# Kernel optimization log

Hardware: AMD Instinct MI355X
Metric: run time of the kernel (lower is better)

Reference implementation:

```python
import jax, jax.numpy as jnp
import numpy as np

D_MODEL = 1024
NUM_HEADS = 16
D_K = D_MODEL // NUM_HEADS
LOCAL_WINDOW = 16
LOCALITY_STRENGTH = 2.0


def _xavier(key, shape):
    fan_in, fan_out = shape[1], shape[0]
    a = jnp.sqrt(6.0 / (fan_in + fan_out))
    return jax.random.uniform(key, shape, jnp.float32, -a, a)


def setup_inputs() -> dict:
    key = jax.random.key(0)
    ks = jax.random.split(key, 9)
    B, S = 4, 2048
    query = jax.random.normal(ks[0], (B, S, D_MODEL), jnp.float32)
    key_t = jax.random.normal(ks[1], (B, S, D_MODEL), jnp.float32)
    value = jax.random.normal(ks[2], (B, S, D_MODEL), jnp.float32)
    wq = _xavier(ks[3], (D_MODEL, D_MODEL))
    wk = _xavier(ks[4], (D_MODEL, D_MODEL))
    wv = _xavier(ks[5], (D_MODEL, D_MODEL))
    wo = _xavier(ks[6], (D_MODEL, D_MODEL))
    bq = jnp.zeros((D_MODEL,), jnp.float32)
    bk = jnp.zeros((D_MODEL,), jnp.float32)
    bv = jnp.zeros((D_MODEL,), jnp.float32)
    bo = jnp.zeros((D_MODEL,), jnp.float32)
    # learned local relative-position bias, length 2*W+1; randomize so grads/math are nontrivial
    local_bias = 0.02 * jax.random.normal(ks[7], (2 * LOCAL_WINDOW + 1,), jnp.float32)
    return {"query": query, "key": key_t, "value": value,
            "wq": wq, "bq": bq, "wk": wk, "bk": bk, "wv": wv, "bv": bv,
            "wo": wo, "bo": bo, "local_bias": local_bias}


def _local_bias_matrix(local_bias, seq_len):
    # bias[i, j] = local_bias[j - i + W] if |j - i| <= W else 0  (banded)
    i = jnp.arange(seq_len)
    rel = i[None, :] - i[:, None]                 # [S, S]
    valid = jnp.abs(rel) <= LOCAL_WINDOW
    idx = jnp.clip(rel + LOCAL_WINDOW, 0, 2 * LOCAL_WINDOW)
    return jnp.where(valid, local_bias[idx], 0.0)  # [S, S]


def reference(query, key, value, wq, bq, wk, bk, wv, bv, wo, bo, local_bias):
    B, S, _ = query.shape
    H, Dk = NUM_HEADS, D_K
    q = (query @ wq.T + bq).reshape(B, S, H, Dk).transpose(0, 2, 1, 3)  # [B,H,S,Dk]
    k = (key @ wk.T + bk).reshape(B, S, H, Dk).transpose(0, 2, 1, 3)
    v = (value @ wv.T + bv).reshape(B, S, H, Dk).transpose(0, 2, 1, 3)
    scores = jnp.einsum('bhqd,bhkd->bhqk', q, k) / jnp.sqrt(jnp.float32(Dk))
    bias = _local_bias_matrix(local_bias, S)       # [S,S], broadcasts over [B,H]
    scores = scores + LOCALITY_STRENGTH * bias
    attn = jax.nn.softmax(scores, axis=-1)
    out = jnp.einsum('bhqk,bhkd->bhqd', attn, v)   # [B,H,S,Dk]
    out = out.transpose(0, 2, 1, 3).reshape(B, S, H * Dk)
    return out @ wo.T + bo
```

## Files before the change

kernel.cpp:

```cpp
#include <hip/hip_runtime.h>
#include <hip/hip_bf16.h>
#include <stdint.h>

typedef __bf16 bf16_t;
typedef bf16_t bf16x8 __attribute__((ext_vector_type(8)));
typedef bf16_t bf16x4 __attribute__((ext_vector_type(4)));
typedef float f32x4 __attribute__((ext_vector_type(4)));

#define LOG2E 1.44269504088896340736f

__device__ __forceinline__ void gld16(const void* g, void* l) {
  __builtin_amdgcn_global_load_lds(
      (__attribute__((address_space(1))) void*)(void*)(g),
      (__attribute__((address_space(3))) void*)(l), 16, 0, 0);
}

__device__ __forceinline__ int swz(int byteoff) {
  return byteoff ^ (((byteoff >> 7) & 7) << 4);
}

__global__ __launch_bounds__(256) void cvt7_kernel(
    const float* __restrict__ a0, const float* __restrict__ a1, const float* __restrict__ a2,
    const float* __restrict__ w0, const float* __restrict__ w1,
    const float* __restrict__ w2, const float* __restrict__ w3,
    bf16_t* __restrict__ e0, bf16_t* __restrict__ e1, bf16_t* __restrict__ e2,
    bf16_t* __restrict__ f0, bf16_t* __restrict__ f1,
    bf16_t* __restrict__ f2, bf16_t* __restrict__ f3) {
  const float* s;
  bf16_t* d;
  int i, stride;
  if (blockIdx.x < 3072) {
    const int t = blockIdx.x >> 10;
    s = (t == 0) ? a0 : ((t == 1) ? a1 : a2);
    d = (t == 0) ? e0 : ((t == 1) ? e1 : e2);
    i = (blockIdx.x & 1023) * 256 + threadIdx.x;
    stride = 1024 * 256;
  } else {
    const int b = blockIdx.x - 3072;
    const int t = b >> 7;
    s = (t == 0) ? w0 : ((t == 1) ? w1 : ((t == 2) ? w2 : w3));
    d = (t == 0) ? f0 : ((t == 1) ? f1 : ((t == 2) ? f2 : f3));
    i = (b & 127) * 256 + threadIdx.x;
    stride = 128 * 256;
  }
#pragma unroll
  for (int u = 0; u < 8; ++u, i += stride) {
    const float4 v = reinterpret_cast<const float4*>(s)[i];
    bf16x4 o;
    o[0] = (bf16_t)v.x; o[1] = (bf16_t)v.y; o[2] = (bf16_t)v.z; o[3] = (bf16_t)v.w;
    reinterpret_cast<bf16x4*>(d)[i] = o;
  }
}

#define GBM 128
#define GBN 128
#define GBK 64

__device__ __forceinline__ void gemm_core(
    const bf16_t* __restrict__ A, const bf16_t* __restrict__ W,
    bf16_t* As, bf16_t* Bs, int m0, int n0, int K,
    int wm, int wn, int rr, int kk8, f32x4 acc[4][4]) {
  const int tid = threadIdx.x;
  const int t16 = tid * 16;
  int srow[4], scb[4];
#pragma unroll
  for (int i = 0; i < 4; ++i) {
    const int so = swz(i * 4096 + t16);
    srow[i] = so >> 7;
    scb[i] = so & 127;
  }
  const char* Ab = (const char*)A;
  const char* Wb = (const char*)W;
  const int nk = K / GBK;

#define GSTAGE(bufsel, kk0)                                                    \
  {                                                                            \
    char* Al = (char*)As + (bufsel) * 16384 + t16;                             \
    char* Bl = (char*)Bs + (bufsel) * 16384 + t16;                             \
    _Pragma("unroll")                                                          \
    for (int i = 0; i < 4; ++i) {                                              \
      gld16(Ab + ((size_t)(m0 + srow[i]) * K + (kk0)) * 2 + scb[i], Al + i * 4096); \
      gld16(Wb + ((size_t)(n0 + srow[i]) * K + (kk0)) * 2 + scb[i], Bl + i * 4096); \
    }                                                                          \
  }

  GSTAGE(0, 0)
  for (int t = 0; t < nk; ++t) {
    const int b = t & 1;
    asm volatile("s_waitcnt vmcnt(0)" ::: "memory");
    __builtin_amdgcn_s_barrier();
    __builtin_amdgcn_sched_barrier(0);
    GSTAGE(b ^ 1, ((t + 1) & (nk - 1)) * GBK)
    const char* Abl = (const char*)As + b * 16384;
    const char* Bbl = (const char*)Bs + b * 16384;
#pragma unroll
    for (int kk = 0; kk < 2; ++kk) {
      bf16x8 a[4], bb[4];
#pragma unroll
      for (int i = 0; i < 4; ++i)
        a[i] = *reinterpret_cast<const bf16x8*>(
            Abl + swz((wm + i * 16 + rr) * 128 + (kk * 32 + kk8) * 2));
#pragma unroll
      for (int i = 0; i < 4; ++i)
        bb[i] = *reinterpret_cast<const bf16x8*>(
            Bbl + swz((wn + i * 16 + rr) * 128 + (kk * 32 + kk8) * 2));
      __builtin_amdgcn_s_setprio(1);
#pragma unroll
      for (int i = 0; i < 4; ++i)
#pragma unroll
        for (int j = 0; j < 4; ++j)
          acc[i][j] = __builtin_amdgcn_mfma_f32_16x16x32_bf16(a[i], bb[j], acc[i][j], 0, 0, 0);
      __builtin_amdgcn_s_setprio(0);
    }
  }
#undef GSTAGE
}

__global__ __launch_bounds__(256) void gemm_qkv(
    const bf16_t* __restrict__ Xq, const bf16_t* __restrict__ Xk, const bf16_t* __restrict__ Xv,
    const bf16_t* __restrict__ Wq, const bf16_t* __restrict__ Wk, const bf16_t* __restrict__ Wv,
    const float* __restrict__ bq, const float* __restrict__ bk, const float* __restrict__ bv,
    bf16_t* __restrict__ Qo, bf16_t* __restrict__ Ko, bf16_t* __restrict__ Vo,
    int M, int N, int K) {
  const int z = blockIdx.z;
  const bf16_t* A = (z == 0) ? Xq : ((z == 1) ? Xk : Xv);
  const bf16_t* W = (z == 0) ? Wq : ((z == 1) ? Wk : Wv);
  const float* bias = (z == 0) ? bq : ((z == 1) ? bk : bv);
  bf16_t* Out = (z == 0) ? Qo : ((z == 1) ? Ko : Vo);

  __shared__ bf16_t As[2 * GBM * GBK];
  __shared__ bf16_t Bs[2 * GBN * GBK];
  const int tid = threadIdx.x;
  const int lane = tid & 63;
  const int w = tid >> 6;
  const int m0 = blockIdx.x * GBM;
  const int n0 = blockIdx.y * GBN;
  const int wm = (w >> 1) * 64;
  const int wn = (w & 1) * 64;
  const int rr = lane & 15;
  const int kk8 = (lane >> 4) * 8;

  f32x4 acc[4][4] = {};
  gemm_core(A, W, As, Bs, m0, n0, K, wm, wn, rr, kk8, acc);

  const int rg = (lane >> 4) * 4;
#pragma unroll
  for (int i = 0; i < 4; ++i) {
#pragma unroll
    for (int j = 0; j < 4; ++j) {
      const int col = n0 + wn + j * 16 + rr;
      const float bi = bias[col];
      if (z == 2) {
        const int row0 = m0 + wm + i * 16 + rg;
        const int b_ = row0 >> 11, s_ = row0 & 2047;
        const int h_ = col >> 6, d_ = col & 63;
        const int k64 = s_ & 63;
        const int sl = (k64 & 32) | ((k64 & 12) << 1) | ((k64 & 16) >> 2);
        const int scol = (s_ & ~63) | sl;
        bf16x4 pack;
#pragma unroll
        for (int r = 0; r < 4; ++r) pack[r] = (bf16_t)(acc[i][j][r] + bi);
        *reinterpret_cast<bf16x4*>(&Out[((size_t)((b_ * 16 + h_) * 64 + d_)) * 2048 + scol]) = pack;
      } else {
        const float scale = (z == 0) ? (0.125f * LOG2E) : 1.0f;
#pragma unroll
        for (int r = 0; r < 4; ++r) {
          const int row = m0 + wm + i * 16 + rg + r;
          const int b_ = row >> 11, s_ = row & 2047;
          const int h_ = col >> 6, d_ = col & 63;
          Out[((size_t)((b_ * 16 + h_) * 2048 + s_)) * 64 + d_] = (bf16_t)((acc[i][j][r] + bi) * scale);
        }
      }
    }
  }
}

__global__ __launch_bounds__(256) void gemm_o(
    const bf16_t* __restrict__ A, const bf16_t* __restrict__ W,
    const float* __restrict__ bias, float* __restrict__ Out,
    int M, int N, int K) {
  __shared__ bf16_t As[2 * GBM * GBK];
  __shared__ bf16_t Bs[2 * GBN * GBK];
  const int tid = threadIdx.x;
  const int lane = tid & 63;
  const int w = tid >> 6;
  const int m0 = blockIdx.x * GBM;
  const int n0 = blockIdx.y * GBN;
  const int wm = (w >> 1) * 64;
  const int wn = (w & 1) * 64;
  const int rr = lane & 15;
  const int kk8 = (lane >> 4) * 8;

  f32x4 acc[4][4] = {};
  gemm_core(A, W, As, Bs, m0, n0, K, wm, wn, rr, kk8, acc);

  const int rg = (lane >> 4) * 4;
#pragma unroll
  for (int i = 0; i < 4; ++i)
#pragma unroll
    for (int j = 0; j < 4; ++j) {
      const int col = n0 + wn + j * 16 + rr;
      const float bi = bias[col];
#pragma unroll
      for (int r = 0; r < 4; ++r) {
        const int row = m0 + wm + i * 16 + rg + r;
        Out[(size_t)row * N + col] = acc[i][j][r] + bi;
      }
    }
}

#define QT 256
#define KT 64

__global__ __launch_bounds__(256, 2) void attn_kernel(
    const bf16_t* __restrict__ Qg, const bf16_t* __restrict__ Kg,
    const bf16_t* __restrict__ Vtg, const float* __restrict__ lb,
    bf16_t* __restrict__ Og) {
  const int S = 2048;
  __shared__ bf16_t Qs[QT * 64];
  __shared__ bf16_t Ks[KT * 64];
  __shared__ bf16_t Vts[64 * KT];
  __shared__ float lbs[33];

  const int tid = threadIdx.x, lane = tid & 63, w = tid >> 6;
  const int bh = blockIdx.x;
  const int qt0 = blockIdx.y * QT;
  const int b_ = bh >> 4, h_ = bh & 15;

  const char* Qb = (const char*)(Qg + (size_t)bh * S * 64);
  const char* Kb = (const char*)(Kg + (size_t)bh * S * 64);
  const char* Vtb = (const char*)(Vtg + (size_t)bh * 64 * S);

#pragma unroll
  for (int i = 0; i < 8; ++i) {
    const int off = i * 4096 + tid * 16;
    gld16(Qb + (size_t)qt0 * 128 + swz(off), (char*)Qs + off);
  }
  if (tid < 33) lbs[tid] = lb[tid];

  const int L0 = tid * 16;
  const int W0 = swz(L0), W1 = swz(L0 + 4096);
  const int vd0 = L0 >> 7, vcb = L0 & 127;
  int4 kr0, kr1, vr0, vr1;

#define LOADKV(t)                                                              \
  {                                                                            \
    const char* kp = Kb + (size_t)(t) * 8192;                                  \
    kr0 = *reinterpret_cast<const int4*>(kp + L0);                             \
    kr1 = *reinterpret_cast<const int4*>(kp + L0 + 4096);                      \
    const char* vp = Vtb + (size_t)(t) * 128;                                  \
    vr0 = *reinterpret_cast<const int4*>(vp + (size_t)vd0 * 4096 + vcb);       \
    vr1 = *reinterpret_cast<const int4*>(vp + (size_t)(vd0 + 32) * 4096 + vcb);\
  }
#define WRITEKV()                                                              \
  {                                                                            \
    *reinterpret_cast<int4*>((char*)Ks + W0) = kr0;                            \
    *reinterpret_cast<int4*>((char*)Ks + W1) = kr1;                            \
    *reinterpret_cast<int4*>((char*)Vts + W0) = vr0;                           \
    *reinterpret_cast<int4*>((char*)Vts + W1) = vr1;                           \
  }

  LOADKV(0)
  __syncthreads();

  const int rr = lane & 15;
  const int kk8 = (lane >> 4) * 8;
  const int rg = (lane >> 4) * 4;

  bf16x8 qf[4][2];
#pragma unroll
  for (int qg = 0; qg < 4; ++qg)
#pragma unroll
    for (int kk = 0; kk < 2; ++kk) {
      const int off = (w * 64 + qg * 16 + rr) * 128 + (kk * 32 + kk8) * 2;
      qf[qg][kk] = *reinterpret_cast<const bf16x8*>((const char*)Qs + swz(off));
    }

  f32x4 oacc[4][4] = {};
  float lrowp[4] = {0.f, 0.f, 0.f, 0.f};

  for (int kt = 0; kt < S / KT; ++kt) {
    WRITEKV()
    __syncthreads();
    LOADKV((kt + 1) & 31)

    bf16x8 kf[4][2];
#pragma unroll
    for (int ni = 0; ni < 4; ++ni)
#pragma unroll
      for (int kk = 0; kk < 2; ++kk) {
        const int off = (ni * 16 + rr) * 128 + (kk * 32 + kk8) * 2;
        kf[ni][kk] = *reinterpret_cast<const bf16x8*>((const char*)Ks + swz(off));
      }
    bf16x8 vf[2][4];
#pragma unroll
    for (int kk = 0; kk < 2; ++kk)
#pragma unroll
      for (int nd = 0; nd < 4; ++nd) {
        const int off = (nd * 16 + rr) * 128 + (kk * 32 + kk8) * 2;
        vf[kk][nd] = *reinterpret_cast<const bf16x8*>((const char*)Vts + swz(off));
      }

    const int kbase = kt * KT;
#pragma unroll
    for (int qg = 0; qg < 4; ++qg) {
      f32x4 sc[4];
      __builtin_amdgcn_s_setprio(1);
#pragma unroll
      for (int ni = 0; ni < 4; ++ni) {
        f32x4 z = {0.f, 0.f, 0.f, 0.f};
#pragma unroll
        for (int kk = 0; kk < 2; ++kk)
          z = __builtin_amdgcn_mfma_f32_16x16x32_bf16(kf[ni][kk], qf[qg][kk], z, 0, 0, 0);
        sc[ni] = z;
      }
      __builtin_amdgcn_s_setprio(0);

      const int qlo = qt0 + w * 64 + qg * 16;
      if (kbase + KT + 16 > qlo && kbase < qlo + 16 + 16) {
        const int q = qlo + rr;
#pragma unroll
        for (int ni = 0; ni < 4; ++ni)
#pragma unroll
          for (int r = 0; r < 4; ++r) {
            const int rel = (kbase + ni * 16 + rg + r) - q;
            if (rel >= -16 && rel <= 16)
              sc[ni][r] += (2.0f * LOG2E) * lbs[rel + 16];
          }
      }

      bf16x8 paf[2];
      float ps0 = 0.f, ps1 = 0.f;
#pragma unroll
      for (int ni = 0; ni < 4; ++ni) {
        const float p0 = __builtin_amdgcn_exp2f(sc[ni][0]);
        const float p1 = __builtin_amdgcn_exp2f(sc[ni][1]);
        const float p2 = __builtin_amdgcn_exp2f(sc[ni][2]);
        const float p3 = __builtin_amdgcn_exp2f(sc[ni][3]);
        ps0 += p0 + p2;
        ps1 += p1 + p3;
        paf[ni >> 1][(ni & 1) * 4 + 0] = (bf16_t)p0;
        paf[ni >> 1][(ni & 1) * 4 + 1] = (bf16_t)p1;
        paf[ni >> 1][(ni & 1) * 4 + 2] = (bf16_t)p2;
        paf[ni >> 1][(ni & 1) * 4 + 3] = (bf16_t)p3;
      }
      lrowp[qg] += ps0 + ps1;

      __builtin_amdgcn_s_setprio(1);
#pragma unroll
      for (int kk = 0; kk < 2; ++kk)
#pragma unroll
        for (int nd = 0; nd < 4; ++nd)
          oacc[qg][nd] = __builtin_amdgcn_mfma_f32_16x16x32_bf16(paf[kk], vf[kk][nd], oacc[qg][nd], 0, 0, 0);
      __builtin_amdgcn_s_setprio(0);
    }
    __syncthreads();
  }

#pragma unroll
  for (int qg = 0; qg < 4; ++qg) {
    float t = lrowp[qg];
    t += __shfl_xor(t, 16, 64);
    t += __shfl_xor(t, 32, 64);
    float lf[4];
#pragma unroll
    for (int r = 0; r < 4; ++r)
      lf[r] = __shfl(t, (lane & 48) | (rg + r), 64);
#pragma unroll
    for (int nd = 0; nd < 4; ++nd)
#pragma unroll
      for (int r = 0; r < 4; ++r) {
        const int srow = qt0 + w * 64 + qg * 16 + rg + r;
        const int d = nd * 16 + rr;
        const float v = oacc[qg][nd][r] / lf[r];
        Og[((size_t)(b_ * 2048 + srow)) * 1024 + h_ * 64 + d] = (bf16_t)v;
      }
  }
}

extern "C" void kernel_launch(void* const* d_in, const int* in_sizes, int n_in,
                              void* d_out, int out_size, void* d_ws, size_t ws_size,
                              hipStream_t stream) {
  const float* q32 = (const float*)d_in[0];
  const float* k32 = (const float*)d_in[1];
  const float* v32 = (const float*)d_in[2];
  const float* wq = (const float*)d_in[3];
  const float* bq = (const float*)d_in[4];
  const float* wk = (const float*)d_in[5];
  const float* bk = (const float*)d_in[6];
  const float* wv = (const float*)d_in[7];
  const float* bv = (const float*)d_in[8];
  const float* wo = (const float*)d_in[9];
  const float* bo = (const float*)d_in[10];
  const float* lb = (const float*)d_in[11];

  const int M = 8192, N = 1024, K = 1024;
  const size_t REG = (size_t)M * N * 2;

  char* ws = (char*)d_ws;
  bf16_t* Xq = (bf16_t*)(ws + 0 * REG);
  bf16_t* Xk = (bf16_t*)(ws + 1 * REG);
  bf16_t* Xv = (bf16_t*)(ws + 2 * REG);
  bf16_t* Qb = (bf16_t*)(ws + 3 * REG);
  bf16_t* Wqb = (bf16_t*)(ws + 4 * REG);
  bf16_t* Wkb = Wqb + (size_t)N * K;
  bf16_t* Wvb = Wkb + (size_t)N * K;
  bf16_t* Wob = Wvb + (size_t)N * K;
  bf16_t* Kb = Xq;
  bf16_t* Vt = Xk;
  bf16_t* attn = Xv;

  cvt7_kernel<<<dim3(3584), dim3(256), 0, stream>>>(
      q32, k32, v32, wq, wk, wv, wo, Xq, Xk, Xv, Wqb, Wkb, Wvb, Wob);

  gemm_qkv<<<dim3(M / GBM, N / GBN, 3), 256, 0, stream>>>(
      Xq, Xk, Xv, Wqb, Wkb, Wvb, bq, bk, bv, Qb, Kb, Vt, M, N, K);

  attn_kernel<<<dim3(64, 2048 / QT), 256, 0, stream>>>(Qb, Kb, Vt, lb, attn);

  gemm_o<<<dim3(M / GBM, N / GBN), 256, 0, stream>>>(attn, Wob, bo, (float*)d_out, M, N, K);
}
```

Before: 196.0 us.

## Fuse fp32-to-bf16 activation conversion into QKV GEMM A-tile loading

The separate conversion pass over the three fp32 activation tensors is removed. The QKV GEMM now loads fp32 A tiles into registers, converts them to bf16 and writes them to swizzled LDS, while W tiles still arrive via global_load_lds. This avoids writing and re-reading roughly 48MB of bf16 intermediates, but each GEMM block reads twice the A bytes, and the register-staged loads add VGPR pressure and a synchronous wait per k-step.

```diff
diff --git a/kernel.cpp b/kernel.cpp
--- a/kernel.cpp
+++ b/kernel.cpp
@@ -19,32 +19,17 @@
   return byteoff ^ (((byteoff >> 7) & 7) << 4);
 }
 
-__global__ __launch_bounds__(256) void cvt7_kernel(
-    const float* __restrict__ a0, const float* __restrict__ a1, const float* __restrict__ a2,
-    const float* __restrict__ w0, const float* __restrict__ w1,
-    const float* __restrict__ w2, const float* __restrict__ w3,
-    bf16_t* __restrict__ e0, bf16_t* __restrict__ e1, bf16_t* __restrict__ e2,
-    bf16_t* __restrict__ f0, bf16_t* __restrict__ f1,
-    bf16_t* __restrict__ f2, bf16_t* __restrict__ f3) {
-  const float* s;
-  bf16_t* d;
-  int i, stride;
-  if (blockIdx.x < 3072) {
-    const int t = blockIdx.x >> 10;
-    s = (t == 0) ? a0 : ((t == 1) ? a1 : a2);
-    d = (t == 0) ? e0 : ((t == 1) ? e1 : e2);
-    i = (blockIdx.x & 1023) * 256 + threadIdx.x;
-    stride = 1024 * 256;
-  } else {
-    const int b = blockIdx.x - 3072;
-    const int t = b >> 7;
-    s = (t == 0) ? w0 : ((t == 1) ? w1 : ((t == 2) ? w2 : w3));
-    d = (t == 0) ? f0 : ((t == 1) ? f1 : ((t == 2) ? f2 : f3));
-    i = (b & 127) * 256 + threadIdx.x;
-    stride = 128 * 256;
-  }
-#pragma unroll
-  for (int u = 0; u < 8; ++u, i += stride) {
+__global__ __launch_bounds__(256) void cvt4_kernel(
+    const float* __restrict__ s0, const float* __restrict__ s1,
+    const float* __restrict__ s2, const float* __restrict__ s3,
+    bf16_t* __restrict__ d0, bf16_t* __restrict__ d1,
+    bf16_t* __restrict__ d2, bf16_t* __restrict__ d3) {
+  const int t = blockIdx.x >> 7;
+  const float* s = (t == 0) ? s0 : ((t == 1) ? s1 : ((t == 2) ? s2 : s3));
+  bf16_t* d = (t == 0) ? d0 : ((t == 1) ? d1 : ((t == 2) ? d2 : d3));
+  int i = (blockIdx.x & 127) * 256 + threadIdx.x;
+#pragma unroll
+  for (int u = 0; u < 8; ++u, i += 128 * 256) {
     const float4 v = reinterpret_cast<const float4*>(s)[i];
     bf16x4 o;
     o[0] = (bf16_t)v.x; o[1] = (bf16_t)v.y; o[2] = (bf16_t)v.z; o[3] = (bf16_t)v.w;
@@ -117,13 +102,13 @@
 }
 
 __global__ __launch_bounds__(256) void gemm_qkv(
-    const bf16_t* __restrict__ Xq, const bf16_t* __restrict__ Xk, const bf16_t* __restrict__ Xv,
+    const float* __restrict__ Xq, const float* __restrict__ Xk, const float* __restrict__ Xv,
     const bf16_t* __restrict__ Wq, const bf16_t* __restrict__ Wk, const bf16_t* __restrict__ Wv,
     const float* __restrict__ bq, const float* __restrict__ bk, const float* __restrict__ bv,
     bf16_t* __restrict__ Qo, bf16_t* __restrict__ Ko, bf16_t* __restrict__ Vo,
     int M, int N, int K) {
   const int z = blockIdx.z;
-  const bf16_t* A = (z == 0) ? Xq : ((z == 1) ? Xk : Xv);
+  const float* A = (z == 0) ? Xq : ((z == 1) ? Xk : Xv);
   const bf16_t* W = (z == 0) ? Wq : ((z == 1) ? Wk : Wv);
   const float* bias = (z == 0) ? bq : ((z == 1) ? bk : bv);
   bf16_t* Out = (z == 0) ? Qo : ((z == 1) ? Ko : Vo);
@@ -140,8 +125,92 @@
   const int rr = lane & 15;
   const int kk8 = (lane >> 4) * 8;
 
+  int arow[4], acelt[4], asw[4];
+#pragma unroll
+  for (int j = 0; j < 4; ++j) {
+    const int lin = tid * 64 + j * 16;
+    asw[j] = swz(lin);
+    arow[j] = lin >> 7;
+    acelt[j] = (lin & 127) >> 1;
+  }
+  const int t16 = tid * 16;
+  int srow[4], scb[4];
+#pragma unroll
+  for (int i = 0; i < 4; ++i) {
+    const int so = swz(i * 4096 + t16);
+    srow[i] = so >> 7;
+    scb[i] = so & 127;
+  }
+  const char* Wb = (const char*)W;
+  const int nk = K / GBK;
+
+  float4 fr[8];
+#define ALOAD(kk0)                                                             \
+  {                                                                            \
+    _Pragma("unroll")                                                          \
+    for (int j = 0; j < 4; ++j) {                                              \
+      const float* ap = A + (size_t)(m0 + arow[j]) * K + (kk0) + acelt[j];     \
+      fr[2 * j] = *reinterpret_cast<const float4*>(ap);                        \
+      fr[2 * j + 1] = *reinterpret_cast<const float4*>(ap + 4);                \
+    }                                                                          \
+  }
+#define BSTAGE(bufsel, kk0)                                                    \
+  {                                                                            \
+    char* Bl = (char*)Bs + (bufsel) * 16384 + t16;                             \
+    _Pragma("unroll")                                                          \
+    for (int i = 0; i < 4; ++i)                                                \
+      gld16(Wb + ((size_t)(n0 + srow[i]) * K + (kk0)) * 2 + scb[i], Bl + i * 4096); \
+  }
+
+  ALOAD(0)
+  BSTAGE(0, 0)
   f32x4 acc[4][4] = {};
-  gemm_core(A, W, As, Bs, m0, n0, K, wm, wn, rr, kk8, acc);
+
+  for (int t = 0; t < nk; ++t) {
+    const int b = t & 1;
+    asm volatile("s_waitcnt vmcnt(0)" ::: "memory");
+    __builtin_amdgcn_s_barrier();
+    __builtin_amdgcn_sched_barrier(0);
+#pragma unroll
+    for (int j = 0; j < 4; ++j) {
+      bf16x8 o;
+      o[0] = (bf16_t)fr[2 * j].x; o[1] = (bf16_t)fr[2 * j].y;
+      o[2] = (bf16_t)fr[2 * j].z; o[3] = (bf16_t)fr[2 * j].w;
+      o[4] = (bf16_t)fr[2 * j + 1].x; o[5] = (bf16_t)fr[2 * j + 1].y;
+      o[6] = (bf16_t)fr[2 * j + 1].z; o[7] = (bf16_t)fr[2 * j + 1].w;
+      *reinterpret_cast<bf16x8*>((char*)As + b * 16384 + asw[j]) = o;
+    }
+    __builtin_amdgcn_sched_barrier(0);
+    const int kn = ((t + 1) & (nk - 1)) * GBK;
+    ALOAD(kn)
+    BSTAGE(b ^ 1, kn)
+    asm volatile("s_waitcnt lgkmcnt(0)" ::: "memory");
+    __builtin_amdgcn_s_barrier();
+    __builtin_amdgcn_sched_barrier(0);
+    const char* Abl = (const char*)As + b * 16384;
+    const char* Bbl = (const char*)Bs + b * 16384;
+#pragma unroll
+    for (int kk = 0; kk < 2; ++kk) {
+      bf16x8 a[4], bb[4];
+#pragma unroll
+      for (int i = 0; i < 4; ++i)
+        a[i] = *reinterpret_cast<const bf16x8*>(
+            Abl + swz((wm + i * 16 + rr) * 128 + (kk * 32 + kk8) * 2));
+#pragma unroll
+      for (int i = 0; i < 4; ++i)
+        bb[i] = *reinterpret_cast<const bf16x8*>(
+            Bbl + swz((wn + i * 16 + rr) * 128 + (kk * 32 + kk8) * 2));
+      __builtin_amdgcn_s_setprio(1);
+#pragma unroll
+      for (int i = 0; i < 4; ++i)
+#pragma unroll
+        for (int j = 0; j < 4; ++j)
+          acc[i][j] = __builtin_amdgcn_mfma_f32_16x16x32_bf16(a[i], bb[j], acc[i][j], 0, 0, 0);
+      __builtin_amdgcn_s_setprio(0);
+    }
+  }
+#undef ALOAD
+#undef BSTAGE
 
   const int rg = (lane >> 4) * 4;
 #pragma unroll
@@ -398,23 +467,20 @@
   const size_t REG = (size_t)M * N * 2;
 
   char* ws = (char*)d_ws;
-  bf16_t* Xq = (bf16_t*)(ws + 0 * REG);
-  bf16_t* Xk = (bf16_t*)(ws + 1 * REG);
-  bf16_t* Xv = (bf16_t*)(ws + 2 * REG);
-  bf16_t* Qb = (bf16_t*)(ws + 3 * REG);
+  bf16_t* Qb = (bf16_t*)(ws + 0 * REG);
+  bf16_t* Kb = (bf16_t*)(ws + 1 * REG);
+  bf16_t* Vt = (bf16_t*)(ws + 2 * REG);
+  bf16_t* attn = (bf16_t*)(ws + 3 * REG);
   bf16_t* Wqb = (bf16_t*)(ws + 4 * REG);
   bf16_t* Wkb = Wqb + (size_t)N * K;
   bf16_t* Wvb = Wkb + (size_t)N * K;
   bf16_t* Wob = Wvb + (size_t)N * K;
-  bf16_t* Kb = Xq;
-  bf16_t* Vt = Xk;
-  bf16_t* attn = Xv;
-
-  cvt7_kernel<<<dim3(3584), dim3(256), 0, stream>>>(
-      q32, k32, v32, wq, wk, wv, wo, Xq, Xk, Xv, Wqb, Wkb, Wvb, Wob);
+
+  cvt4_kernel<<<dim3(512), dim3(256), 0, stream>>>(
+      wq, wk, wv, wo, Wqb, Wkb, Wvb, Wob);
 
   gemm_qkv<<<dim3(M / GBM, N / GBN, 3), 256, 0, stream>>>(
-      Xq, Xk, Xv, Wqb, Wkb, Wvb, bq, bk, bv, Qb, Kb, Vt, M, N, K);
+      q32, k32, v32, Wqb, Wkb, Wvb, bq, bk, bv, Qb, Kb, Vt, M, N, K);
 
   attn_kernel<<<dim3(64, 2048 / QT), 256, 0, stream>>>(Qb, Kb, Vt, lb, attn);
 
```

New measurement: 248.4 us. 1.27x slower.

## Double-buffer K/V tiles in LDS with direct global-to-LDS async loads

Applied to the files above, without the earlier changes.

Replaces the register-staged K/V prefetch (global load into registers, then an LDS store) with a two-slot LDS ring filled by global_load_lds, which writes global memory straight into LDS. Each iteration waits on vmcnt, passes one barrier, and issues the next tile into the other buffer, so the trailing __syncthreads is dropped. This saves registers and the explicit LDS store instructions. In exchange it doubles the K/V LDS footprint, which could limit occupancy with two blocks per CU, and the vmcnt(0) wait sits right before compute, so the prefetch gets little time to hide latency.

```diff
diff --git a/kernel.cpp b/kernel.cpp
--- a/kernel.cpp
+++ b/kernel.cpp
@@ -218,8 +218,7 @@
     bf16_t* __restrict__ Og) {
   const int S = 2048;
   __shared__ bf16_t Qs[QT * 64];
-  __shared__ bf16_t Ks[KT * 64];
-  __shared__ bf16_t Vts[64 * KT];
+  __shared__ char KVs[2][16384];
   __shared__ float lbs[33];
 
   const int tid = threadIdx.x, lane = tid & 63, w = tid >> 6;
@@ -236,31 +235,25 @@
     const int off = i * 4096 + tid * 16;
     gld16(Qb + (size_t)qt0 * 128 + swz(off), (char*)Qs + off);
   }
+
+  const int L0 = tid * 16;
+  const int sk0 = swz(L0), sk1 = swz(L0 + 4096);
+  const int vd0 = sk0 >> 7, vc0 = sk0 & 127;
+  const int vd1 = sk1 >> 7, vc1 = sk1 & 127;
+
+#define STAGEKV(bufsel, t)                                                     \
+  {                                                                            \
+    char* base = KVs[bufsel];                                                  \
+    const char* kp = Kb + (size_t)(t) * 8192;                                  \
+    gld16(kp + sk0, base + L0);                                                \
+    gld16(kp + sk1, base + L0 + 4096);                                         \
+    const char* vp = Vtb + (size_t)(t) * 128;                                  \
+    gld16(vp + (size_t)vd0 * 4096 + vc0, base + 8192 + L0);                    \
+    gld16(vp + (size_t)vd1 * 4096 + vc1, base + 8192 + L0 + 4096);             \
+  }
+
+  STAGEKV(0, 0)
   if (tid < 33) lbs[tid] = lb[tid];
-
-  const int L0 = tid * 16;
-  const int W0 = swz(L0), W1 = swz(L0 + 4096);
-  const int vd0 = L0 >> 7, vcb = L0 & 127;
-  int4 kr0, kr1, vr0, vr1;
-
-#define LOADKV(t)                                                              \
-  {                                                                            \
-    const char* kp = Kb + (size_t)(t) * 8192;                                  \
-    kr0 = *reinterpret_cast<const int4*>(kp + L0);                             \
-    kr1 = *reinterpret_cast<const int4*>(kp + L0 + 4096);                      \
-    const char* vp = Vtb + (size_t)(t) * 128;                                  \
-    vr0 = *reinterpret_cast<const int4*>(vp + (size_t)vd0 * 4096 + vcb);       \
-    vr1 = *reinterpret_cast<const int4*>(vp + (size_t)(vd0 + 32) * 4096 + vcb);\
-  }
-#define WRITEKV()                                                              \
-  {                                                                            \
-    *reinterpret_cast<int4*>((char*)Ks + W0) = kr0;                            \
-    *reinterpret_cast<int4*>((char*)Ks + W1) = kr1;                            \
-    *reinterpret_cast<int4*>((char*)Vts + W0) = vr0;                           \
-    *reinterpret_cast<int4*>((char*)Vts + W1) = vr1;                           \
-  }
-
-  LOADKV(0)
   __syncthreads();
 
   const int rr = lane & 15;
@@ -280,9 +273,13 @@
   float lrowp[4] = {0.f, 0.f, 0.f, 0.f};
 
   for (int kt = 0; kt < S / KT; ++kt) {
-    WRITEKV()
-    __syncthreads();
-    LOADKV((kt + 1) & 31)
+    asm volatile("s_waitcnt vmcnt(0)" ::: "memory");
+    __builtin_amdgcn_s_barrier();
+    __builtin_amdgcn_sched_barrier(0);
+    STAGEKV((kt + 1) & 1, (kt + 1) & 31)
+
+    const char* KsB = KVs[kt & 1];
+    const char* VsB = KsB + 8192;
 
     bf16x8 kf[4][2];
 #pragma unroll
@@ -290,7 +287,7 @@
 #pragma unroll
       for (int kk = 0; kk < 2; ++kk) {
         const int off = (ni * 16 + rr) * 128 + (kk * 32 + kk8) * 2;
-        kf[ni][kk] = *reinterpret_cast<const bf16x8*>((const char*)Ks + swz(off));
+        kf[ni][kk] = *reinterpret_cast<const bf16x8*>(KsB + swz(off));
       }
     bf16x8 vf[2][4];
 #pragma unroll
@@ -298,7 +295,7 @@
 #pragma unroll
       for (int nd = 0; nd < 4; ++nd) {
         const int off = (nd * 16 + rr) * 128 + (kk * 32 + kk8) * 2;
-        vf[kk][nd] = *reinterpret_cast<const bf16x8*>((const char*)Vts + swz(off));
+        vf[kk][nd] = *reinterpret_cast<const bf16x8*>(VsB + swz(off));
       }
 
     const int kbase = kt * KT;
@@ -354,8 +351,8 @@
           oacc[qg][nd] = __builtin_amdgcn_mfma_f32_16x16x32_bf16(paf[kk], vf[kk][nd], oacc[qg][nd], 0, 0, 0);
       __builtin_amdgcn_s_setprio(0);
     }
-    __syncthreads();
-  }
+  }
+#undef STAGEKV
 
 #pragma unroll
   for (int qg = 0; qg < 4; ++qg) {
```

Result: no change. 196.1 us (+0.0%).
